# Performance work log

Hardware: AMD Instinct MI355X
Metric: run time of the kernel (lower is better)

The kernel has to match this reference:

```python
import math
import jax, jax.numpy as jnp
import numpy as np

B, LD, LE = 8, 512, 512
D, H, DK, F, L, V = 1024, 16, 64, 4096, 3, 32000
EPS = 1e-5
NEG = -1000000000.0


def setup_inputs() -> dict:
    key = jax.random.key(0)
    ks = jax.random.split(key, 16)
    s = 0.02
    dec_inputs = jax.random.randint(ks[0], (B, LD), 0, V)
    # causal mask: True = masked out (matches masked_fill semantics)
    self_mask = jnp.broadcast_to(jnp.triu(jnp.ones((LD, LD), bool), k=1), (B, LD, LD))
    enc_output = jax.random.normal(ks[1], (B, LE, D), jnp.float32)
    encoder_mask = jnp.zeros((B, LD, LE), bool)  # no encoder padding
    embed = jax.random.normal(ks[2], (V, D), jnp.float32) * s
    # sinusoidal positional encoding, pe[:LD]
    pos = jnp.arange(LD, dtype=jnp.float32)[:, None]
    div = jnp.exp(jnp.arange(0, D, 2, dtype=jnp.float32) * (-math.log(10000.0) / D))
    pe = jnp.zeros((LD, D), jnp.float32)
    pe = pe.at[:, 0::2].set(jnp.sin(pos * div)).at[:, 1::2].set(jnp.cos(pos * div))
    # per-layer params; axis 1 of attn params: 0=self-attn, 1=enc-dec attn
    wq = jax.random.normal(ks[3], (L, 2, D, D), jnp.float32) * s
    wk = jax.random.normal(ks[4], (L, 2, D, D), jnp.float32) * s
    wv = jax.random.normal(ks[5], (L, 2, D, D), jnp.float32) * s
    wo = jax.random.normal(ks[6], (L, 2, D, D), jnp.float32) * s
    bq = jnp.zeros((L, 2, D), jnp.float32)
    bk = jnp.zeros((L, 2, D), jnp.float32)
    bv = jnp.zeros((L, 2, D), jnp.float32)
    bo = jnp.zeros((L, 2, D), jnp.float32)
    ffn_w1 = jax.random.normal(ks[7], (L, F, D), jnp.float32) * s
    ffn_b1 = jnp.zeros((L, F), jnp.float32)
    ffn_w2 = jax.random.normal(ks[8], (L, D, F), jnp.float32) * s
    ffn_b2 = jnp.zeros((L, D), jnp.float32)
    ln_g = jnp.ones((L, 3, D), jnp.float32)   # norm1/2/3 gains
    ln_b = jnp.zeros((L, 3, D), jnp.float32)  # norm1/2/3 biases
    return dict(dec_inputs=dec_inputs, self_mask=self_mask, enc_output=enc_output,
                encoder_mask=encoder_mask, embed=embed, pe=pe,
                wq=wq, bq=bq, wk=wk, bk=bk, wv=wv, bv=bv, wo=wo, bo=bo,
                ffn_w1=ffn_w1, ffn_b1=ffn_b1, ffn_w2=ffn_w2, ffn_b2=ffn_b2,
                ln_g=ln_g, ln_b=ln_b)


def _ln(x, g, b):
    m = jnp.mean(x, axis=-1, keepdims=True)
    v = jnp.mean((x - m) ** 2, axis=-1, keepdims=True)
    return (x - m) * jax.lax.rsqrt(v + EPS) * g + b


def _mha(qi, ki, vi, mask, wq, bq, wk, bk, wv, bv, wo, bo):
    Bq, Lq, _ = qi.shape
    Lk = ki.shape[1]
    Q = (qi @ wq.T + bq).reshape(Bq, Lq, H, DK).transpose(0, 2, 1, 3)
    K = (ki @ wk.T + bk).reshape(Bq, Lk, H, DK).transpose(0, 2, 1, 3)
    Vv = (vi @ wv.T + bv).reshape(Bq, Lk, H, DK).transpose(0, 2, 1, 3)
    scores = jnp.einsum('bhqd,bhkd->bhqk', Q, K) / math.sqrt(DK)
    scores = jnp.where(mask[:, None, :, :], NEG, scores)
    attn = jax.nn.softmax(scores, axis=-1)
    ctx = jnp.einsum('bhqk,bhkd->bhqd', attn, Vv)
    ctx = ctx.transpose(0, 2, 1, 3).reshape(Bq, Lq, H * DK)
    return ctx @ wo.T + bo


def reference(dec_inputs, self_mask, enc_output, encoder_mask, embed, pe,
              wq, bq, wk, bk, wv, bv, wo, bo,
              ffn_w1, ffn_b1, ffn_w2, ffn_b2, ln_g, ln_b):
    x = embed[dec_inputs] * math.sqrt(D) + pe[None, :, :]
    for l in range(L):
        h = _ln(x, ln_g[l, 0], ln_b[l, 0])
        a = _mha(h, h, h, self_mask,
                 wq[l, 0], bq[l, 0], wk[l, 0], bk[l, 0], wv[l, 0], bv[l, 0], wo[l, 0], bo[l, 0])
        x = x + a
        h = _ln(x, ln_g[l, 1], ln_b[l, 1])
        c = _mha(h, enc_output, enc_output, encoder_mask,
                 wq[l, 1], bq[l, 1], wk[l, 1], bk[l, 1], wv[l, 1], bv[l, 1], wo[l, 1], bo[l, 1])
        x = x + c
        h = _ln(x, ln_g[l, 2], ln_b[l, 2])
        f = jax.nn.relu(h @ ffn_w1[l].T + ffn_b1[l]) @ ffn_w2[l].T + ffn_b2[l]
        # faithful quirk of the source: residual is the cross-attn output, not x
        x = c + f
    return x
```

## Files before the change

kernel.cpp:

```cpp
#include <hip/hip_runtime.h>
#include <hip/hip_bf16.h>

using bf16x8 = __attribute__((ext_vector_type(8))) short;
using f32x4  = __attribute__((ext_vector_type(4))) float;
using u16x4  = __attribute__((ext_vector_type(4))) unsigned short;

#define DEVI static __device__ __forceinline__
#define SBAR() asm volatile("s_barrier" ::: "memory")

DEVI unsigned short f2b(float f) {
  unsigned int u = __float_as_uint(f);
  u += 0x7FFFu + ((u >> 16) & 1u);
  return (unsigned short)(u >> 16);
}

DEVI void gload16(const unsigned short* g, unsigned short* l) {
  __builtin_amdgcn_global_load_lds(
      (const __attribute__((address_space(1))) unsigned int*)g,
      (__attribute__((address_space(3))) unsigned int*)l, 16, 0, 0);
}

DEVI float wred_max16(float v) {
#pragma unroll
  for (int m = 1; m < 16; m <<= 1) v = fmaxf(v, __shfl_xor(v, m, 64));
  return v;
}
DEVI float wred_sum16(float v) {
#pragma unroll
  for (int m = 1; m < 16; m <<= 1) v += __shfl_xor(v, m, 64);
  return v;
}


__global__ void cvt_kernel(const float* __restrict__ in,
                           unsigned short* __restrict__ out, int n4) {
  int i = blockIdx.x * blockDim.x + threadIdx.x;
  const int stride = gridDim.x * blockDim.x;
  for (; i < n4; i += stride) {
    const float4 v = ((const float4*)in)[i];
    u16x4 o;
    o[0] = f2b(v.x); o[1] = f2b(v.y); o[2] = f2b(v.z); o[3] = f2b(v.w);
    ((u16x4*)out)[i] = o;
  }
}

__global__ void pack_w(const float* __restrict__ s0,
                       const float* __restrict__ s1,
                       const float* __restrict__ s2,
                       int sub, unsigned short* __restrict__ dst, int nm) {
  const int r = blockIdx.x;
  const int m = blockIdx.y;
  const int l = blockIdx.z;
  const float* src = (m == 0 ? s0 : m == 1 ? s1 : s2)
                   + (size_t)(l * 2 + sub) * 1048576 + (size_t)r * 1024;
  unsigned short* d = dst + ((size_t)(l * nm + m) * 1024 + r) * 1024;
  const int col = threadIdx.x * 4;
  const float4 v = *(const float4*)(src + col);
  u16x4 o;
  o[0] = f2b(v.x); o[1] = f2b(v.y); o[2] = f2b(v.z); o[3] = f2b(v.w);
  *(u16x4*)(d + col) = o;
}

__global__ void pack_bias(const float* __restrict__ s0,
                          const float* __restrict__ s1,
                          const float* __restrict__ s2,
                          int sub, float* __restrict__ dst, int nm) {
  const int m = blockIdx.x, l = blockIdx.y;
  const float* src = (m == 0 ? s0 : m == 1 ? s1 : s2) + (size_t)(l * 2 + sub) * 1024;
  float* d = dst + ((size_t)l * nm + m) * 1024;
  const int i = threadIdx.x * 4;
  *(float4*)(d + i) = *(const float4*)(src + i);
}

__global__ void embed_kernel(const int* __restrict__ ids,
                             const float* __restrict__ emb,
                             const float* __restrict__ pe,
                             float* __restrict__ x) {
  const int row = blockIdx.x;
  const int t = row & 511;
  const int col = threadIdx.x * 4;
  const int id = ids[row];
  const float4 e = *(const float4*)(emb + (size_t)id * 1024 + col);
  const float4 p = *(const float4*)(pe + (size_t)t * 1024 + col);
  float4 o;
  o.x = e.x * 32.f + p.x; o.y = e.y * 32.f + p.y;
  o.z = e.z * 32.f + p.z; o.w = e.w * 32.f + p.w;
  *(float4*)(x + (size_t)row * 1024 + col) = o;
}

__global__ void ln_kernel(const float* __restrict__ x,
                          const float* __restrict__ g,
                          const float* __restrict__ b,
                          unsigned short* __restrict__ out) {
  const int row = blockIdx.x;
  const int l = threadIdx.x;
  const float4* xr = (const float4*)(x + (size_t)row * 1024);
  float4 v[4];
  float s = 0.f;
#pragma unroll
  for (int i = 0; i < 4; ++i) {
    v[i] = xr[l * 4 + i];
    s += v[i].x + v[i].y + v[i].z + v[i].w;
  }
#pragma unroll
  for (int m = 1; m < 64; m <<= 1) s += __shfl_xor(s, m, 64);
  const float mean = s * (1.f / 1024.f);
  float vs = 0.f;
#pragma unroll
  for (int i = 0; i < 4; ++i) {
    float dx = v[i].x - mean, dy = v[i].y - mean, dz = v[i].z - mean, dw = v[i].w - mean;
    vs += dx * dx + dy * dy + dz * dz + dw * dw;
  }
#pragma unroll
  for (int m = 1; m < 64; m <<= 1) vs += __shfl_xor(vs, m, 64);
  const float inv = rsqrtf(vs * (1.f / 1024.f) + 1e-5f);
#pragma unroll
  for (int i = 0; i < 4; ++i) {
    const int col = l * 16 + i * 4;
    const float4 gg = *(const float4*)(g + col);
    const float4 bb = *(const float4*)(b + col);
    u16x4 o;
    o[0] = f2b((v[i].x - mean) * inv * gg.x + bb.x);
    o[1] = f2b((v[i].y - mean) * inv * gg.y + bb.y);
    o[2] = f2b((v[i].z - mean) * inv * gg.z + bb.z);
    o[3] = f2b((v[i].w - mean) * inv * gg.w + bb.w);
    *(u16x4*)(out + (size_t)row * 1024 + col) = o;
  }
}

__global__ void vt_kernel(const unsigned short* __restrict__ Vsrc, int vsd,
                          unsigned short* __restrict__ Vt) {
  __shared__ alignas(16) unsigned short t[64][72];
  const int tt = blockIdx.x;
  const int h  = blockIdx.y;
  const int b  = blockIdx.z;
  const int tid = threadIdx.x;
  const int r  = tid >> 2;
  const int ch = tid & 3;
  const unsigned short* src =
      Vsrc + (size_t)(b * 512 + tt * 64 + r) * vsd + (size_t)h * 64 + ch * 16;
  const bf16x8 v0 = *(const bf16x8*)src;
  const bf16x8 v1 = *(const bf16x8*)(src + 8);
#pragma unroll
  for (int j = 0; j < 8; ++j) {
    t[ch * 16 + j][r]     = (unsigned short)v0[j];
    t[ch * 16 + 8 + j][r] = (unsigned short)v1[j];
  }
  __syncthreads();
  const int d  = tid >> 2;
  const int tp = tid & 3;
  unsigned short* dst = Vt + (((size_t)(b * 16 + h) * 64 + d) * 512) + tt * 64 + tp * 16;
  *(bf16x8*)dst       = *(const bf16x8*)&t[d][tp * 16];
  *(bf16x8*)(dst + 8) = *(const bf16x8*)&t[d][tp * 16 + 8];
}


template<int EPI>
__global__ __launch_bounds__(512, 1) void gemm8p(
    const unsigned short* __restrict__ A,
    const unsigned short* __restrict__ Bw,
    const float* __restrict__ bias,
    int N, unsigned short* __restrict__ out0) {
  constexpr int K = 1024, NT = 16;
  __shared__ alignas(16) unsigned short AsE[256 * 64];
  __shared__ alignas(16) unsigned short BsE[256 * 64];
  __shared__ alignas(16) unsigned short AsO[256 * 64];
  __shared__ alignas(16) unsigned short BsO[256 * 64];
  const int tid = threadIdx.x;
  const int lane = tid & 63;
  const int wave = tid >> 6;
  const int wr = wave >> 2;
  const int wc = wave & 3;
  int id = blockIdx.x;
  const int nwg = gridDim.x;
  id = (id & 7) * (nwg >> 3) + (id >> 3);
  const int nn = N >> 8;
  const int bx = id % nn;
  const int by = id / nn;
  const int m0 = by * 256;
  const int n0 = bx * 256;
  const int ro = lane & 15;
  const int hi = lane >> 4;

  auto stA = [&](unsigned short* buf, int q, int kt) {
    const int row = tid >> 3;
    const int lc = (tid & 7) ^ (row & 7);
    gload16(A + (size_t)(m0 + q * 64 + row) * K + (size_t)kt * 64 + lc * 8,
            buf + q * 4096 + tid * 8);
  };
  auto stB = [&](unsigned short* buf, int q, int kt) {
    const int row = tid >> 3;
    const int lc = (tid & 7) ^ (row & 7);
    gload16(Bw + (size_t)(n0 + q * 64 + row) * K + (size_t)kt * 64 + lc * 8,
            buf + q * 4096 + tid * 8);
  };

  f32x4 acc[8][4];
#pragma unroll
  for (int i = 0; i < 8; ++i)
#pragma unroll
    for (int j = 0; j < 4; ++j) acc[i][j] = f32x4{0.f, 0.f, 0.f, 0.f};

  bf16x8 af[4][2], bfL[2][2], bfR[2][2];

  auto ldAL = [&](const unsigned short* buf) {
#pragma unroll
    for (int mi = 0; mi < 4; ++mi) {
      const int r = wr * 128 + mi * 16 + ro;
#pragma unroll
      for (int ks = 0; ks < 2; ++ks)
        af[mi][ks] = *(const bf16x8*)&buf[r * 64 + (((ks << 2) + hi) ^ (r & 7)) * 8];
    }
  };
  auto ldAH = [&](const unsigned short* buf) {
#pragma unroll
    for (int mi = 0; mi < 4; ++mi) {
      const int r = wr * 128 + 64 + mi * 16 + ro;
#pragma unroll
      for (int ks = 0; ks < 2; ++ks)
        af[mi][ks] = *(const bf16x8*)&buf[r * 64 + (((ks << 2) + hi) ^ (r & 7)) * 8];
    }
  };
  auto ldBL = [&](const unsigned short* buf) {
#pragma unroll
    for (int nj = 0; nj < 2; ++nj) {
      const int r = wc * 64 + nj * 16 + ro;
#pragma unroll
      for (int ks = 0; ks < 2; ++ks)
        bfL[nj][ks] = *(const bf16x8*)&buf[r * 64 + (((ks << 2) + hi) ^ (r & 7)) * 8];
    }
  };
  auto ldBR = [&](const unsigned short* buf) {
#pragma unroll
    for (int nj = 0; nj < 2; ++nj) {
      const int r = wc * 64 + 32 + nj * 16 + ro;
#pragma unroll
      for (int ks = 0; ks < 2; ++ks)
        bfR[nj][ks] = *(const bf16x8*)&buf[r * 64 + (((ks << 2) + hi) ^ (r & 7)) * 8];
    }
  };
  auto mmQ = [&](bf16x8 (&bf)[2][2], int mo, int no) {
    __builtin_amdgcn_s_setprio(1);
#pragma unroll
    for (int ks = 0; ks < 2; ++ks)
#pragma unroll
      for (int mi = 0; mi < 4; ++mi)
#pragma unroll
        for (int nj = 0; nj < 2; ++nj)
          acc[mo + mi][no + nj] =
              __builtin_amdgcn_mfma_f32_16x16x32_bf16(af[mi][ks], bf[nj][ks],
                                                      acc[mo + mi][no + nj], 0, 0, 0);
    __builtin_amdgcn_s_setprio(0);
  };

  stA(AsE, 0, 0); stA(AsE, 1, 0); stA(AsE, 2, 0); stA(AsE, 3, 0);
  stB(BsE, 0, 0); stB(BsE, 1, 0); stB(BsE, 2, 0); stB(BsE, 3, 0);
  stA(AsO, 0, 1); stA(AsO, 1, 1); stA(AsO, 2, 1); stA(AsO, 3, 1);
  stB(BsO, 0, 1); stB(BsO, 1, 1);
  asm volatile("s_waitcnt vmcnt(0)" ::: "memory");
  SBAR();

  for (int t = 0; t < NT; t += 2) {
    const bool last = (t + 2 >= NT);
    ldAL(AsE); ldBL(BsE);
    stB(BsO, 2, t + 1); stB(BsO, 3, t + 1);
    SBAR(); mmQ(bfL, 0, 0); SBAR();
    ldBR(BsE);
    if (!last) { stA(AsE, 0, t + 2); stA(AsE, 2, t + 2); }
    SBAR(); mmQ(bfR, 0, 2); SBAR();
    ldAH(AsE);
    if (!last) { stB(BsE, 0, t + 2); stB(BsE, 1, t + 2); }
    SBAR(); mmQ(bfL, 4, 0); SBAR();
    if (!last) {
      stA(AsE, 1, t + 2); stA(AsE, 3, t + 2);
      asm volatile("s_waitcnt vmcnt(6)" ::: "memory");
    } else {
      asm volatile("s_waitcnt vmcnt(0)" ::: "memory");
    }
    SBAR(); mmQ(bfR, 4, 2); SBAR();
    ldAL(AsO); ldBL(BsO);
    if (!last) { stB(BsE, 2, t + 2); stB(BsE, 3, t + 2); }
    SBAR(); mmQ(bfL, 0, 0); SBAR();
    ldBR(BsO);
    if (!last) { stA(AsO, 0, t + 3); stA(AsO, 2, t + 3); }
    SBAR(); mmQ(bfR, 0, 2); SBAR();
    ldAH(AsO);
    if (!last) { stB(BsO, 0, t + 3); stB(BsO, 1, t + 3); }
    SBAR(); mmQ(bfL, 4, 0); SBAR();
    if (!last) {
      stA(AsO, 1, t + 3); stA(AsO, 3, t + 3);
      asm volatile("s_waitcnt vmcnt(6)" ::: "memory");
    }
    SBAR(); mmQ(bfR, 4, 2); SBAR();
  }

  const int r4 = hi * 4;
#pragma unroll
  for (int mi = 0; mi < 8; ++mi) {
#pragma unroll
    for (int nj = 0; nj < 4; ++nj) {
      const int cg = n0 + wc * 64 + nj * 16 + ro;
      const float bv = bias[cg];
#pragma unroll
      for (int q = 0; q < 4; ++q) {
        const int rg = m0 + wr * 128 + mi * 16 + r4 + q;
        const float v = acc[mi][nj][q] + bv;
        out0[(size_t)rg * N + cg] = f2b(EPI == 1 ? fmaxf(v, 0.f) : v);
      }
    }
  }
}


enum { EPI_BF16 = 0, EPI_RELU_BF16 = 1, EPI_RES = 2, EPI_RES2 = 3 };

template<int EPI, int BM, int BN>
__global__ void gemm_bt(const unsigned short* __restrict__ A,
                        const unsigned short* __restrict__ Bw,
                        const float* __restrict__ bias,
                        int N, int K, int nn,
                        void* out0, const float* res, float* out1) {
  constexpr int MI = BM / 32;
  constexpr int NJ = BN / 32;
  __shared__ alignas(16) unsigned short As[2][BM * 64];
  __shared__ alignas(16) unsigned short Bs[2][BN * 64];
  const int tid = threadIdx.x;
  const int lane = tid & 63;
  const int wave = tid >> 6;
  int id = blockIdx.x;
  const int nwg = gridDim.x;
  id = (id & 7) * (nwg >> 3) + (id >> 3);
  const int bx = id % nn;
  const int by = id / nn;
  const int m0 = by * BM;
  const int n0 = bx * BN;
  const int wm = (wave >> 1) * (BM / 2);
  const int wn = (wave & 1) * (BN / 2);

  auto stage = [&](int buf, int kt) {
    const size_t k0 = (size_t)kt * 64;
#pragma unroll
    for (int i = 0; i < MI; ++i) {
      const int c = tid + 256 * i;
      const int row = c >> 3;
      const int lc = (c & 7) ^ (row & 7);
      gload16(A + (size_t)(m0 + row) * K + k0 + lc * 8, &As[buf][c * 8]);
    }
#pragma unroll
    for (int i = 0; i < NJ; ++i) {
      const int c = tid + 256 * i;
      const int row = c >> 3;
      const int lc = (c & 7) ^ (row & 7);
      gload16(Bw + (size_t)(n0 + row) * K + k0 + lc * 8, &Bs[buf][c * 8]);
    }
  };

  f32x4 acc[MI][NJ];
#pragma unroll
  for (int i = 0; i < MI; ++i)
#pragma unroll
    for (int j = 0; j < NJ; ++j) acc[i][j] = f32x4{0.f, 0.f, 0.f, 0.f};

  const int nk = K >> 6;
  stage(0, 0);
  int cur = 0;
  const int ro = lane & 15;
  const int hi = lane >> 4;
  for (int kt = 0; kt < nk; ++kt) {
    __syncthreads();
    if (kt + 1 < nk) stage(cur ^ 1, kt + 1);
    bf16x8 af[MI][2], bf[NJ][2];
#pragma unroll
    for (int i = 0; i < MI; ++i) {
      const int r = wm + i * 16 + ro;
#pragma unroll
      for (int ks = 0; ks < 2; ++ks)
        af[i][ks] = *(const bf16x8*)&As[cur][r * 64 + (((ks << 2) + hi) ^ (r & 7)) * 8];
    }
#pragma unroll
    for (int j = 0; j < NJ; ++j) {
      const int r = wn + j * 16 + ro;
#pragma unroll
      for (int ks = 0; ks < 2; ++ks)
        bf[j][ks] = *(const bf16x8*)&Bs[cur][r * 64 + (((ks << 2) + hi) ^ (r & 7)) * 8];
    }
#pragma unroll
    for (int ks = 0; ks < 2; ++ks)
#pragma unroll
      for (int i = 0; i < MI; ++i)
#pragma unroll
        for (int j = 0; j < NJ; ++j)
          acc[i][j] = __builtin_amdgcn_mfma_f32_16x16x32_bf16(af[i][ks], bf[j][ks], acc[i][j], 0, 0, 0);
    cur ^= 1;
  }

  const int r4 = hi * 4;
#pragma unroll
  for (int i = 0; i < MI; ++i) {
#pragma unroll
    for (int j = 0; j < NJ; ++j) {
      const int cg = n0 + wn + j * 16 + ro;
      const float bv = bias[cg];
#pragma unroll
      for (int q = 0; q < 4; ++q) {
        const int rg = m0 + wm + i * 16 + r4 + q;
        const size_t idx = (size_t)rg * N + cg;
        const float v = acc[i][j][q] + bv;
        if (EPI == EPI_BF16) {
          ((unsigned short*)out0)[idx] = f2b(v);
        } else if (EPI == EPI_RELU_BF16) {
          ((unsigned short*)out0)[idx] = f2b(fmaxf(v, 0.f));
        } else if (EPI == EPI_RES) {
          ((float*)out0)[idx] = res[idx] + v;
        } else {
          const float r = res[idx];
          ((float*)out0)[idx] = v;
          out1[idx] = r + v;
        }
      }
    }
  }
}


template<bool CAUSAL>
__global__ __launch_bounds__(256) void attn_kernel(
    const unsigned short* __restrict__ Qg, int qs,
    const unsigned short* __restrict__ Kg, int ksd,
    const unsigned short* __restrict__ Vt,
    unsigned short* __restrict__ Og) {
  __shared__ alignas(16) unsigned short Ks[2][64 * 64];
  __shared__ alignas(16) unsigned short Vs[2][64 * 64];
  __shared__ alignas(16) unsigned short Pl[4][32 * 64];
  const int qt0 = blockIdx.x;
  const int h  = blockIdx.y;
  const int b  = blockIdx.z;
  const int tid = threadIdx.x;
  const int lane = tid & 63;
  const int w = tid >> 6;
  const int ro = lane & 15;
  const int hi = lane >> 4;
  const int qrow0 = qt0 * 128 + w * 32;
  const size_t qbase = (size_t)b * 512 * qs  + (size_t)h * 64;
  const size_t kbase = (size_t)b * 512 * ksd + (size_t)h * 64;
  const size_t vbase = ((size_t)(b * 16 + h)) * 64 * 512;
  const size_t obase = (size_t)b * 512 * 1024 + (size_t)h * 64;

  bf16x8 qf[2][2];
#pragma unroll
  for (int mi = 0; mi < 2; ++mi)
#pragma unroll
    for (int ks = 0; ks < 2; ++ks)
      qf[mi][ks] = *(const bf16x8*)&Qg[qbase + (size_t)(qrow0 + mi * 16 + ro) * qs + ks * 32 + hi * 8];

  f32x4 o[2][4];
  float mrun[2][4], lrun[2][4];
#pragma unroll
  for (int mi = 0; mi < 2; ++mi) {
#pragma unroll
    for (int di = 0; di < 4; ++di) o[mi][di] = f32x4{0.f, 0.f, 0.f, 0.f};
#pragma unroll
    for (int q = 0; q < 4; ++q) { mrun[mi][q] = -1e30f; lrun[mi][q] = 0.f; }
  }

  auto stage = [&](int buf, int kt) {
#pragma unroll
    for (int i = 0; i < 2; ++i) {
      const int c = tid + 256 * i;
      const int row = c >> 3;
      const int lc = (c & 7) ^ (row & 7);
      gload16(Kg + kbase + (size_t)(kt * 64 + row) * ksd + lc * 8, &Ks[buf][c * 8]);
    }
#pragma unroll
    for (int i = 0; i < 2; ++i) {
      const int c = tid + 256 * i;
      const int row = c >> 3;
      const int lc = (c & 7) ^ (row & 7);
      gload16(Vt + vbase + (size_t)row * 512 + (size_t)kt * 64 + lc * 8, &Vs[buf][c * 8]);
    }
  };

  const int ktmax = CAUSAL ? (qt0 * 2 + 1) : 7;
  stage(0, 0);
  int cur = 0;
  for (int kt = 0; kt <= ktmax; ++kt) {
    __syncthreads();
    if (kt < ktmax) stage(cur ^ 1, kt + 1);
    const bool skip = CAUSAL && (kt * 64 > qrow0 + 31);
    if (!skip) {
      bf16x8 kf[4][2];
#pragma unroll
      for (int ni = 0; ni < 4; ++ni) {
        const int r = ni * 16 + ro;
#pragma unroll
        for (int ks = 0; ks < 2; ++ks)
          kf[ni][ks] = *(const bf16x8*)&Ks[cur][r * 64 + (((ks << 2) + hi) ^ (r & 7)) * 8];
      }

      f32x4 s[2][4];
#pragma unroll
      for (int mi = 0; mi < 2; ++mi)
#pragma unroll
        for (int ni = 0; ni < 4; ++ni) s[mi][ni] = f32x4{0.f, 0.f, 0.f, 0.f};
#pragma unroll
      for (int ks = 0; ks < 2; ++ks)
#pragma unroll
        for (int mi = 0; mi < 2; ++mi)
#pragma unroll
          for (int ni = 0; ni < 4; ++ni)
            s[mi][ni] = __builtin_amdgcn_mfma_f32_16x16x32_bf16(qf[mi][ks], kf[ni][ks], s[mi][ni], 0, 0, 0);

      const bool dm = CAUSAL && (kt * 64 + 63 > qrow0);
#pragma unroll
      for (int mi = 0; mi < 2; ++mi)
#pragma unroll
        for (int ni = 0; ni < 4; ++ni)
#pragma unroll
          for (int q = 0; q < 4; ++q) {
            float e = s[mi][ni][q] * 0.125f;
            if (dm && (kt * 64 + ni * 16 + ro) > (qrow0 + mi * 16 + hi * 4 + q)) e = -1e9f;
            s[mi][ni][q] = e;
          }

      float fac[2][4];
#pragma unroll
      for (int mi = 0; mi < 2; ++mi)
#pragma unroll
        for (int q = 0; q < 4; ++q) {
          float rm = s[mi][0][q];
#pragma unroll
          for (int ni = 1; ni < 4; ++ni) rm = fmaxf(rm, s[mi][ni][q]);
          rm = wred_max16(rm);
          const float mn = fmaxf(mrun[mi][q], rm);
          fac[mi][q] = __expf(mrun[mi][q] - mn);
          mrun[mi][q] = mn;
        }
#pragma unroll
      for (int mi = 0; mi < 2; ++mi)
#pragma unroll
        for (int q = 0; q < 4; ++q) {
          float rs = 0.f;
#pragma unroll
          for (int ni = 0; ni < 4; ++ni) {
            const float pv = __expf(s[mi][ni][q] - mrun[mi][q]);
            s[mi][ni][q] = pv;
            rs += pv;
          }
          rs = wred_sum16(rs);
          lrun[mi][q] = lrun[mi][q] * fac[mi][q] + rs;
        }
#pragma unroll
      for (int mi = 0; mi < 2; ++mi)
#pragma unroll
        for (int di = 0; di < 4; ++di)
#pragma unroll
          for (int q = 0; q < 4; ++q) o[mi][di][q] *= fac[mi][q];

#pragma unroll
      for (int mi = 0; mi < 2; ++mi)
#pragma unroll
        for (int ni = 0; ni < 4; ++ni)
#pragma unroll
          for (int q = 0; q < 4; ++q) {
            const int row = mi * 16 + hi * 4 + q;
            const int col = ni * 16 + ro;
            const int sc  = ((col >> 3) ^ (row & 7)) * 8 + (col & 7);
            Pl[w][row * 64 + sc] = f2b(s[mi][ni][q]);
          }

      bf16x8 pa[2][2];
#pragma unroll
      for (int mi = 0; mi < 2; ++mi)
#pragma unroll
        for (int ks = 0; ks < 2; ++ks) {
          const int row = mi * 16 + ro;
          pa[mi][ks] = *(const bf16x8*)&Pl[w][row * 64 + (((ks << 2) + hi) ^ (row & 7)) * 8];
        }

#pragma unroll
      for (int di = 0; di < 4; ++di)
#pragma unroll
        for (int ks = 0; ks < 2; ++ks) {
          const int r = di * 16 + ro;
          const bf16x8 vf = *(const bf16x8*)&Vs[cur][r * 64 + (((ks << 2) + hi) ^ (r & 7)) * 8];
#pragma unroll
          for (int mi = 0; mi < 2; ++mi)
            o[mi][di] = __builtin_amdgcn_mfma_f32_16x16x32_bf16(pa[mi][ks], vf, o[mi][di], 0, 0, 0);
        }
    }
    cur ^= 1;
  }

#pragma unroll
  for (int mi = 0; mi < 2; ++mi)
#pragma unroll
    for (int di = 0; di < 4; ++di)
#pragma unroll
      for (int q = 0; q < 4; ++q) {
        const float val = o[mi][di][q] / lrun[mi][q];
        Og[obase + (size_t)(qrow0 + mi * 16 + hi * 4 + q) * 1024 + di * 16 + ro] = f2b(val);
      }
}


extern "C" void kernel_launch(void* const* d_in, const int* in_sizes, int n_in,
                              void* d_out, int out_size, void* d_ws, size_t ws_size,
                              hipStream_t stream) {
  (void)in_sizes; (void)n_in; (void)out_size; (void)ws_size;
  const int*   dec = (const int*)d_in[0];
  const float* enc = (const float*)d_in[2];
  const float* emb = (const float*)d_in[4];
  const float* pe  = (const float*)d_in[5];
  const float* wq  = (const float*)d_in[6];
  const float* bq  = (const float*)d_in[7];
  const float* wk  = (const float*)d_in[8];
  const float* bk  = (const float*)d_in[9];
  const float* wv  = (const float*)d_in[10];
  const float* bv  = (const float*)d_in[11];
  const float* wo  = (const float*)d_in[12];
  const float* bo  = (const float*)d_in[13];
  const float* w1  = (const float*)d_in[14];
  const float* b1  = (const float*)d_in[15];
  const float* w2  = (const float*)d_in[16];
  const float* b2  = (const float*)d_in[17];
  const float* lng = (const float*)d_in[18];
  const float* lnb = (const float*)d_in[19];

  const size_t SZ_ACT = 4194304ull;

  char* p = (char*)d_ws;
  auto alloc = [&](size_t bytes) { char* r = p; p += (bytes + 255) & ~(size_t)255; return r; };
  unsigned short* qkvw  = (unsigned short*)alloc(3ull * 3 * 1048576 * 2);
  unsigned short* kvw   = (unsigned short*)alloc(3ull * 2 * 1048576 * 2);
  unsigned short* wqxb  = (unsigned short*)alloc(3ull * 1048576 * 2);
  unsigned short* Wob   = (unsigned short*)alloc(6291456ull * 2);
  unsigned short* W1b   = (unsigned short*)alloc(12582912ull * 2);
  unsigned short* W2b   = (unsigned short*)alloc(12582912ull * 2);
  unsigned short* encb  = (unsigned short*)alloc(SZ_ACT * 2);
  float*          x     = (float*)alloc(SZ_ACT * 4);
  float*          c     = (float*)alloc(SZ_ACT * 4);
  unsigned short* hb    = (unsigned short*)alloc(SZ_ACT * 2);
  unsigned short* qkvb  = (unsigned short*)alloc(4096ull * 3072 * 2);
  unsigned short* kvb   = (unsigned short*)alloc(4096ull * 6144 * 2);
  unsigned short* qb    = (unsigned short*)alloc(SZ_ACT * 2);
  unsigned short* vtb   = (unsigned short*)alloc(SZ_ACT * 2);
  unsigned short* mid   = (unsigned short*)alloc(4096ull * 4096 * 2);
  float*          qkvbias = (float*)alloc(3ull * 3072 * 4);
  float*          kvbias  = (float*)alloc(3ull * 2048 * 4);

  cvt_kernel<<<2048, 256, 0, stream>>>(wo, Wob, 1572864);
  cvt_kernel<<<2048, 256, 0, stream>>>(w1, W1b, 3145728);
  cvt_kernel<<<2048, 256, 0, stream>>>(w2, W2b, 3145728);
  cvt_kernel<<<2048, 256, 0, stream>>>(enc, encb, 1048576);
  pack_w<<<dim3(1024, 3, 3), 256, 0, stream>>>(wq, wk, wv, 0, qkvw, 3);
  pack_w<<<dim3(1024, 2, 3), 256, 0, stream>>>(wk, wv, wv, 1, kvw, 2);
  pack_w<<<dim3(1024, 1, 3), 256, 0, stream>>>(wq, wq, wq, 1, wqxb, 1);
  pack_bias<<<dim3(3, 3), 256, 0, stream>>>(bq, bk, bv, 0, qkvbias, 3);
  pack_bias<<<dim3(2, 3), 256, 0, stream>>>(bk, bv, bv, 1, kvbias, 2);
  embed_kernel<<<4096, 256, 0, stream>>>(dec, emb, pe, x);

  gemm8p<0><<<16 * 24, 512, 0, stream>>>(encb, kvw, kvbias, 6144, kvb);

  const dim3 gAttn(4, 16, 8);
  const dim3 gVt(8, 16, 8);

  for (int l = 0; l < 3; ++l) {
    const float* g0 = lng + (l * 3 + 0) * 1024; const float* e0 = lnb + (l * 3 + 0) * 1024;
    const float* g1 = lng + (l * 3 + 1) * 1024; const float* e1 = lnb + (l * 3 + 1) * 1024;
    const float* g2 = lng + (l * 3 + 2) * 1024; const float* e2 = lnb + (l * 3 + 2) * 1024;

    ln_kernel<<<4096, 64, 0, stream>>>(x, g0, e0, hb);
    gemm8p<0><<<16 * 12, 512, 0, stream>>>(hb, qkvw + (size_t)l * 3 * 1048576,
        qkvbias + l * 3072, 3072, qkvb);
    vt_kernel<<<gVt, 256, 0, stream>>>(qkvb + 2048, 3072, vtb);
    attn_kernel<true><<<gAttn, 256, 0, stream>>>(qkvb, 3072, qkvb + 1024, 3072, vtb, hb);
    gemm_bt<EPI_RES, 128, 64><<<32 * 16, 256, 0, stream>>>(hb, Wob + (size_t)(l * 2) * 1048576,
        bo + (l * 2) * 1024, 1024, 1024, 16, x, x, nullptr);

    ln_kernel<<<4096, 64, 0, stream>>>(x, g1, e1, hb);
    gemm_bt<EPI_BF16, 128, 64><<<32 * 16, 256, 0, stream>>>(hb, wqxb + (size_t)l * 1048576,
        bq + (l * 2 + 1) * 1024, 1024, 1024, 16, qb, nullptr, nullptr);
    vt_kernel<<<gVt, 256, 0, stream>>>(kvb + l * 2048 + 1024, 6144, vtb);
    attn_kernel<false><<<gAttn, 256, 0, stream>>>(qb, 1024, kvb + l * 2048, 6144, vtb, hb);
    gemm_bt<EPI_RES2, 128, 64><<<32 * 16, 256, 0, stream>>>(hb, Wob + (size_t)(l * 2 + 1) * 1048576,
        bo + (l * 2 + 1) * 1024, 1024, 1024, 16, c, x, x);

    ln_kernel<<<4096, 64, 0, stream>>>(x, g2, e2, hb);
    gemm8p<1><<<16 * 16, 512, 0, stream>>>(hb, W1b + (size_t)l * 4194304,
        b1 + l * 4096, 4096, mid);
    float* xout = (l == 2) ? (float*)d_out : x;
    gemm_bt<EPI_RES, 128, 64><<<32 * 16, 256, 0, stream>>>(mid, W2b + (size_t)l * 4194304,
        b2 + l * 1024, 1024, 4096, 16, xout, c, nullptr);
  }
}
```

Measured before the change: 1.112 ms.

## Split-K the FFN down-projection with the 256x256 GEMM and a reduce kernel

Moves the FFN second GEMM (K=4096, N=1024) from the smaller gemm_bt tile kernel onto the large 256x256 pipelined gemm8p core. It uses a 4-way split-K so the grid fills 256 workgroups. Each split writes fp32 partials to a new buffer, and a separate reduce kernel sums them with the bias and the residual. This adds a 64 MB fp32 partial write and read plus an extra launch in exchange for the higher-throughput GEMM core.

Result: faster. 1.073 ms (-3.6%).

```diff
diff --git a/kernel.cpp b/kernel.cpp
--- a/kernel.cpp
+++ b/kernel.cpp
@@ -155,54 +155,37 @@
 }
 
 
-template<int EPI>
-__global__ __launch_bounds__(512, 1) void gemm8p(
-    const unsigned short* __restrict__ A,
-    const unsigned short* __restrict__ Bw,
-    const float* __restrict__ bias,
-    int N, unsigned short* __restrict__ out0) {
-  constexpr int K = 1024, NT = 16;
-  __shared__ alignas(16) unsigned short AsE[256 * 64];
-  __shared__ alignas(16) unsigned short BsE[256 * 64];
-  __shared__ alignas(16) unsigned short AsO[256 * 64];
-  __shared__ alignas(16) unsigned short BsO[256 * 64];
-  const int tid = threadIdx.x;
+struct G8POut { f32x4 acc[8][4]; int m0, n0, wr, wc, ro, hi; };
+
+template<int LDA, int LDB>
+DEVI void gemm8p_core(const unsigned short* __restrict__ A,
+                      const unsigned short* __restrict__ Bw,
+                      int m0, int n0, int kofs,
+                      unsigned short* AsE, unsigned short* BsE,
+                      unsigned short* AsO, unsigned short* BsO,
+                      int tid, f32x4 (&acc)[8][4]) {
+  constexpr int NT = 16;
   const int lane = tid & 63;
   const int wave = tid >> 6;
   const int wr = wave >> 2;
   const int wc = wave & 3;
-  int id = blockIdx.x;
-  const int nwg = gridDim.x;
-  id = (id & 7) * (nwg >> 3) + (id >> 3);
-  const int nn = N >> 8;
-  const int bx = id % nn;
-  const int by = id / nn;
-  const int m0 = by * 256;
-  const int n0 = bx * 256;
   const int ro = lane & 15;
   const int hi = lane >> 4;
 
   auto stA = [&](unsigned short* buf, int q, int kt) {
     const int row = tid >> 3;
     const int lc = (tid & 7) ^ (row & 7);
-    gload16(A + (size_t)(m0 + q * 64 + row) * K + (size_t)kt * 64 + lc * 8,
+    gload16(A + (size_t)(m0 + q * 64 + row) * LDA + kofs + kt * 64 + lc * 8,
             buf + q * 4096 + tid * 8);
   };
   auto stB = [&](unsigned short* buf, int q, int kt) {
     const int row = tid >> 3;
     const int lc = (tid & 7) ^ (row & 7);
-    gload16(Bw + (size_t)(n0 + q * 64 + row) * K + (size_t)kt * 64 + lc * 8,
+    gload16(Bw + (size_t)(n0 + q * 64 + row) * LDB + kofs + kt * 64 + lc * 8,
             buf + q * 4096 + tid * 8);
   };
 
-  f32x4 acc[8][4];
-#pragma unroll
-  for (int i = 0; i < 8; ++i)
-#pragma unroll
-    for (int j = 0; j < 4; ++j) acc[i][j] = f32x4{0.f, 0.f, 0.f, 0.f};
-
   bf16x8 af[4][2], bfL[2][2], bfR[2][2];
-
   auto ldAL = [&](const unsigned short* buf) {
 #pragma unroll
     for (int mi = 0; mi < 4; ++mi) {
@@ -293,7 +276,40 @@
     }
     SBAR(); mmQ(bfR, 4, 2); SBAR();
   }
-
+}
+
+template<int EPI>
+__global__ __launch_bounds__(512, 1) void gemm8p(
+    const unsigned short* __restrict__ A,
+    const unsigned short* __restrict__ Bw,
+    const float* __restrict__ bias,
+    int N, unsigned short* __restrict__ out0) {
+  __shared__ alignas(16) unsigned short AsE[256 * 64];
+  __shared__ alignas(16) unsigned short BsE[256 * 64];
+  __shared__ alignas(16) unsigned short AsO[256 * 64];
+  __shared__ alignas(16) unsigned short BsO[256 * 64];
+  const int tid = threadIdx.x;
+  int id = blockIdx.x;
+  const int nwg = gridDim.x;
+  id = (id & 7) * (nwg >> 3) + (id >> 3);
+  const int nn = N >> 8;
+  const int bx = id % nn;
+  const int by = id / nn;
+  const int m0 = by * 256;
+  const int n0 = bx * 256;
+
+  f32x4 acc[8][4];
+#pragma unroll
+  for (int i = 0; i < 8; ++i)
+#pragma unroll
+    for (int j = 0; j < 4; ++j) acc[i][j] = f32x4{0.f, 0.f, 0.f, 0.f};
+
+  gemm8p_core<1024, 1024>(A, Bw, m0, n0, 0, AsE, BsE, AsO, BsO, tid, acc);
+
+  const int lane = tid & 63;
+  const int wave = tid >> 6;
+  const int wr = wave >> 2, wc = wave & 3;
+  const int ro = lane & 15, hi = lane >> 4;
   const int r4 = hi * 4;
 #pragma unroll
   for (int mi = 0; mi < 8; ++mi) {
@@ -308,6 +324,79 @@
         out0[(size_t)rg * N + cg] = f2b(EPI == 1 ? fmaxf(v, 0.f) : v);
       }
     }
+  }
+}
+
+__global__ __launch_bounds__(512, 1) void gemm_sk8(
+    const unsigned short* __restrict__ A,
+    const unsigned short* __restrict__ Bw,
+    float* __restrict__ pbuf) {
+  __shared__ alignas(16) unsigned short AsE[256 * 64];
+  __shared__ alignas(16) unsigned short BsE[256 * 64];
+  __shared__ alignas(16) unsigned short AsO[256 * 64];
+  __shared__ alignas(16) unsigned short BsO[256 * 64];
+  const int tid = threadIdx.x;
+  int id = blockIdx.x;
+  const int nwg = gridDim.x;
+  id = (id & 7) * (nwg >> 3) + (id >> 3);
+  const int s  = id >> 6;
+  const int r6 = id & 63;
+  const int bx = r6 & 3;
+  const int by = r6 >> 2;
+  const int m0 = by * 256;
+  const int n0 = bx * 256;
+
+  f32x4 acc[8][4];
+#pragma unroll
+  for (int i = 0; i < 8; ++i)
+#pragma unroll
+    for (int j = 0; j < 4; ++j) acc[i][j] = f32x4{0.f, 0.f, 0.f, 0.f};
+
+  gemm8p_core<4096, 4096>(A, Bw, m0, n0, s * 1024, AsE, BsE, AsO, BsO, tid, acc);
+
+  float* out = pbuf + (size_t)s * 4096 * 1024;
+  const int lane = tid & 63;
+  const int wave = tid >> 6;
+  const int wr = wave >> 2, wc = wave & 3;
+  const int ro = lane & 15, hi = lane >> 4;
+  const int r4 = hi * 4;
+#pragma unroll
+  for (int mi = 0; mi < 8; ++mi)
+#pragma unroll
+    for (int nj = 0; nj < 4; ++nj) {
+      const int cg = n0 + wc * 64 + nj * 16 + ro;
+#pragma unroll
+      for (int q = 0; q < 4; ++q) {
+        const int rg = m0 + wr * 128 + mi * 16 + r4 + q;
+        out[(size_t)rg * 1024 + cg] = acc[mi][nj][q];
+      }
+    }
+}
+
+__global__ void reduce4_kernel(const float* __restrict__ c,
+                               const float* __restrict__ pbuf,
+                               const float* __restrict__ bias,
+                               float* __restrict__ xout) {
+  const int n4 = 4096 * 1024 / 4;
+  int i = blockIdx.x * blockDim.x + threadIdx.x;
+  const int stride = gridDim.x * blockDim.x;
+  const float4* p0 = (const float4*)pbuf;
+  const float4* p1 = (const float4*)(pbuf + 4194304);
+  const float4* p2 = (const float4*)(pbuf + 2 * 4194304);
+  const float4* p3 = (const float4*)(pbuf + 3 * 4194304);
+  for (; i < n4; i += stride) {
+    const float4 cc = ((const float4*)c)[i];
+    const float4 a0 = p0[i];
+    const float4 a1 = p1[i];
+    const float4 a2 = p2[i];
+    const float4 a3 = p3[i];
+    const float4 bb = ((const float4*)bias)[i & 255];
+    float4 o;
+    o.x = cc.x + (a0.x + a1.x) + (a2.x + a3.x) + bb.x;
+    o.y = cc.y + (a0.y + a1.y) + (a2.y + a3.y) + bb.y;
+    o.z = cc.z + (a0.z + a1.z) + (a2.z + a3.z) + bb.z;
+    o.w = cc.w + (a0.w + a1.w) + (a2.w + a3.w) + bb.w;
+    ((float4*)xout)[i] = o;
   }
 }
 
@@ -645,6 +734,7 @@
   unsigned short* qb    = (unsigned short*)alloc(SZ_ACT * 2);
   unsigned short* vtb   = (unsigned short*)alloc(SZ_ACT * 2);
   unsigned short* mid   = (unsigned short*)alloc(4096ull * 4096 * 2);
+  float*          pbuf  = (float*)alloc(4ull * SZ_ACT * 4);
   float*          qkvbias = (float*)alloc(3ull * 3072 * 4);
   float*          kvbias  = (float*)alloc(3ull * 2048 * 4);
 
@@ -688,8 +778,8 @@
     ln_kernel<<<4096, 64, 0, stream>>>(x, g2, e2, hb);
     gemm8p<1><<<16 * 16, 512, 0, stream>>>(hb, W1b + (size_t)l * 4194304,
         b1 + l * 4096, 4096, mid);
+    gemm_sk8<<<256, 512, 0, stream>>>(mid, W2b + (size_t)l * 4194304, pbuf);
     float* xout = (l == 2) ? (float*)d_out : x;
-    gemm_bt<EPI_RES, 128, 64><<<32 * 16, 256, 0, stream>>>(mid, W2b + (size_t)l * 4194304,
-        b2 + l * 1024, 1024, 4096, 16, xout, c, nullptr);
-  }
-}
+    reduce4_kernel<<<2048, 256, 0, stream>>>(c, pbuf, b2 + l * 1024, xout);
+  }
+}
```

## Replace N=1024 GEMMs with 128x128 ping-pong pipelined 8-wave kernel

Applied to the files above, without the earlier changes.

Replaces the simple double-buffered 128x64 gemm_bt used for the output projections, cross-attention Q projection and FFN down-projection with a new gemm4p kernel. The new kernel uses 128x128 tiles, 512 threads, even/odd LDS buffers, interleaved async global-to-LDS loads with explicit vmcnt waits and barriers, and raised wave priority around the MFMA blocks. gemm8p is also split into a reusable core function with a K offset parameter, though that path is not yet used elsewhere. The goal is better overlap of memory and MFMA work and more data reuse per tile, at the cost of fewer workgroups (256) on a large-CU GPU.

New measurement: 1.115 ms. About the same (+0.3%).

```diff
diff --git a/kernel.cpp b/kernel.cpp
--- a/kernel.cpp
+++ b/kernel.cpp
@@ -155,54 +155,35 @@
 }
 
 
-template<int EPI>
-__global__ __launch_bounds__(512, 1) void gemm8p(
-    const unsigned short* __restrict__ A,
-    const unsigned short* __restrict__ Bw,
-    const float* __restrict__ bias,
-    int N, unsigned short* __restrict__ out0) {
-  constexpr int K = 1024, NT = 16;
-  __shared__ alignas(16) unsigned short AsE[256 * 64];
-  __shared__ alignas(16) unsigned short BsE[256 * 64];
-  __shared__ alignas(16) unsigned short AsO[256 * 64];
-  __shared__ alignas(16) unsigned short BsO[256 * 64];
-  const int tid = threadIdx.x;
+template<int LDA, int LDB>
+DEVI void gemm8p_core(const unsigned short* __restrict__ A,
+                      const unsigned short* __restrict__ Bw,
+                      int m0, int n0, int kofs,
+                      unsigned short* AsE, unsigned short* BsE,
+                      unsigned short* AsO, unsigned short* BsO,
+                      int tid, f32x4 (&acc)[8][4]) {
+  constexpr int NT = 16;
   const int lane = tid & 63;
   const int wave = tid >> 6;
   const int wr = wave >> 2;
   const int wc = wave & 3;
-  int id = blockIdx.x;
-  const int nwg = gridDim.x;
-  id = (id & 7) * (nwg >> 3) + (id >> 3);
-  const int nn = N >> 8;
-  const int bx = id % nn;
-  const int by = id / nn;
-  const int m0 = by * 256;
-  const int n0 = bx * 256;
   const int ro = lane & 15;
   const int hi = lane >> 4;
 
   auto stA = [&](unsigned short* buf, int q, int kt) {
     const int row = tid >> 3;
     const int lc = (tid & 7) ^ (row & 7);
-    gload16(A + (size_t)(m0 + q * 64 + row) * K + (size_t)kt * 64 + lc * 8,
+    gload16(A + (size_t)(m0 + q * 64 + row) * LDA + kofs + kt * 64 + lc * 8,
             buf + q * 4096 + tid * 8);
   };
   auto stB = [&](unsigned short* buf, int q, int kt) {
     const int row = tid >> 3;
     const int lc = (tid & 7) ^ (row & 7);
-    gload16(Bw + (size_t)(n0 + q * 64 + row) * K + (size_t)kt * 64 + lc * 8,
+    gload16(Bw + (size_t)(n0 + q * 64 + row) * LDB + kofs + kt * 64 + lc * 8,
             buf + q * 4096 + tid * 8);
   };
 
-  f32x4 acc[8][4];
-#pragma unroll
-  for (int i = 0; i < 8; ++i)
-#pragma unroll
-    for (int j = 0; j < 4; ++j) acc[i][j] = f32x4{0.f, 0.f, 0.f, 0.f};
-
   bf16x8 af[4][2], bfL[2][2], bfR[2][2];
-
   auto ldAL = [&](const unsigned short* buf) {
 #pragma unroll
     for (int mi = 0; mi < 4; ++mi) {
@@ -293,7 +274,40 @@
     }
     SBAR(); mmQ(bfR, 4, 2); SBAR();
   }
-
+}
+
+template<int EPI>
+__global__ __launch_bounds__(512, 1) void gemm8p(
+    const unsigned short* __restrict__ A,
+    const unsigned short* __restrict__ Bw,
+    const float* __restrict__ bias,
+    int N, unsigned short* __restrict__ out0) {
+  __shared__ alignas(16) unsigned short AsE[256 * 64];
+  __shared__ alignas(16) unsigned short BsE[256 * 64];
+  __shared__ alignas(16) unsigned short AsO[256 * 64];
+  __shared__ alignas(16) unsigned short BsO[256 * 64];
+  const int tid = threadIdx.x;
+  int id = blockIdx.x;
+  const int nwg = gridDim.x;
+  id = (id & 7) * (nwg >> 3) + (id >> 3);
+  const int nn = N >> 8;
+  const int bx = id % nn;
+  const int by = id / nn;
+  const int m0 = by * 256;
+  const int n0 = bx * 256;
+
+  f32x4 acc[8][4];
+#pragma unroll
+  for (int i = 0; i < 8; ++i)
+#pragma unroll
+    for (int j = 0; j < 4; ++j) acc[i][j] = f32x4{0.f, 0.f, 0.f, 0.f};
+
+  gemm8p_core<1024, 1024>(A, Bw, m0, n0, 0, AsE, BsE, AsO, BsO, tid, acc);
+
+  const int lane = tid & 63;
+  const int wave = tid >> 6;
+  const int wr = wave >> 2, wc = wave & 3;
+  const int ro = lane & 15, hi = lane >> 4;
   const int r4 = hi * 4;
 #pragma unroll
   for (int mi = 0; mi < 8; ++mi) {
@@ -314,98 +328,131 @@
 
 enum { EPI_BF16 = 0, EPI_RELU_BF16 = 1, EPI_RES = 2, EPI_RES2 = 3 };
 
-template<int EPI, int BM, int BN>
-__global__ void gemm_bt(const unsigned short* __restrict__ A,
-                        const unsigned short* __restrict__ Bw,
-                        const float* __restrict__ bias,
-                        int N, int K, int nn,
-                        void* out0, const float* res, float* out1) {
-  constexpr int MI = BM / 32;
-  constexpr int NJ = BN / 32;
-  __shared__ alignas(16) unsigned short As[2][BM * 64];
-  __shared__ alignas(16) unsigned short Bs[2][BN * 64];
+template<int EPI>
+__global__ __launch_bounds__(512, 2) void gemm4p(
+    const unsigned short* __restrict__ A,
+    const unsigned short* __restrict__ Bw,
+    const float* __restrict__ bias,
+    int N, int K, int nn,
+    void* out0, const float* res, float* out1) {
+  __shared__ alignas(16) unsigned short AsE[128 * 64];
+  __shared__ alignas(16) unsigned short BsE[128 * 64];
+  __shared__ alignas(16) unsigned short AsO[128 * 64];
+  __shared__ alignas(16) unsigned short BsO[128 * 64];
   const int tid = threadIdx.x;
   const int lane = tid & 63;
   const int wave = tid >> 6;
+  const int wr = wave >> 1;
+  const int wc = wave & 1;
   int id = blockIdx.x;
   const int nwg = gridDim.x;
   id = (id & 7) * (nwg >> 3) + (id >> 3);
   const int bx = id % nn;
   const int by = id / nn;
-  const int m0 = by * BM;
-  const int n0 = bx * BN;
-  const int wm = (wave >> 1) * (BM / 2);
-  const int wn = (wave & 1) * (BN / 2);
-
-  auto stage = [&](int buf, int kt) {
-    const size_t k0 = (size_t)kt * 64;
-#pragma unroll
-    for (int i = 0; i < MI; ++i) {
-      const int c = tid + 256 * i;
-      const int row = c >> 3;
-      const int lc = (c & 7) ^ (row & 7);
-      gload16(A + (size_t)(m0 + row) * K + k0 + lc * 8, &As[buf][c * 8]);
-    }
-#pragma unroll
-    for (int i = 0; i < NJ; ++i) {
-      const int c = tid + 256 * i;
-      const int row = c >> 3;
-      const int lc = (c & 7) ^ (row & 7);
-      gload16(Bw + (size_t)(n0 + row) * K + k0 + lc * 8, &Bs[buf][c * 8]);
-    }
-  };
-
-  f32x4 acc[MI][NJ];
-#pragma unroll
-  for (int i = 0; i < MI; ++i)
-#pragma unroll
-    for (int j = 0; j < NJ; ++j) acc[i][j] = f32x4{0.f, 0.f, 0.f, 0.f};
-
-  const int nk = K >> 6;
-  stage(0, 0);
-  int cur = 0;
+  const int m0 = by * 128;
+  const int n0 = bx * 128;
   const int ro = lane & 15;
   const int hi = lane >> 4;
-  for (int kt = 0; kt < nk; ++kt) {
-    __syncthreads();
-    if (kt + 1 < nk) stage(cur ^ 1, kt + 1);
-    bf16x8 af[MI][2], bf[NJ][2];
-#pragma unroll
-    for (int i = 0; i < MI; ++i) {
-      const int r = wm + i * 16 + ro;
+
+  auto stA = [&](unsigned short* buf, int h, int kt) {
+    const int row = tid >> 3;
+    const int lc = (tid & 7) ^ (row & 7);
+    gload16(A + (size_t)(m0 + h * 64 + row) * K + (size_t)kt * 64 + lc * 8,
+            buf + h * 4096 + tid * 8);
+  };
+  auto stB = [&](unsigned short* buf, int h, int kt) {
+    const int row = tid >> 3;
+    const int lc = (tid & 7) ^ (row & 7);
+    gload16(Bw + (size_t)(n0 + h * 64 + row) * K + (size_t)kt * 64 + lc * 8,
+            buf + h * 4096 + tid * 8);
+  };
+
+  f32x4 acc[2][4];
+#pragma unroll
+  for (int i = 0; i < 2; ++i)
+#pragma unroll
+    for (int j = 0; j < 4; ++j) acc[i][j] = f32x4{0.f, 0.f, 0.f, 0.f};
+
+  bf16x8 af[2][2], bfL[2][2], bfR[2][2];
+  auto ldA = [&](const unsigned short* buf) {
+#pragma unroll
+    for (int mi = 0; mi < 2; ++mi) {
+      const int r = wr * 32 + mi * 16 + ro;
 #pragma unroll
       for (int ks = 0; ks < 2; ++ks)
-        af[i][ks] = *(const bf16x8*)&As[cur][r * 64 + (((ks << 2) + hi) ^ (r & 7)) * 8];
-    }
-#pragma unroll
-    for (int j = 0; j < NJ; ++j) {
-      const int r = wn + j * 16 + ro;
+        af[mi][ks] = *(const bf16x8*)&buf[r * 64 + (((ks << 2) + hi) ^ (r & 7)) * 8];
+    }
+  };
+  auto ldBL = [&](const unsigned short* buf) {
+#pragma unroll
+    for (int nj = 0; nj < 2; ++nj) {
+      const int r = wc * 64 + nj * 16 + ro;
 #pragma unroll
       for (int ks = 0; ks < 2; ++ks)
-        bf[j][ks] = *(const bf16x8*)&Bs[cur][r * 64 + (((ks << 2) + hi) ^ (r & 7)) * 8];
-    }
+        bfL[nj][ks] = *(const bf16x8*)&buf[r * 64 + (((ks << 2) + hi) ^ (r & 7)) * 8];
+    }
+  };
+  auto ldBR = [&](const unsigned short* buf) {
+#pragma unroll
+    for (int nj = 0; nj < 2; ++nj) {
+      const int r = wc * 64 + 32 + nj * 16 + ro;
+#pragma unroll
+      for (int ks = 0; ks < 2; ++ks)
+        bfR[nj][ks] = *(const bf16x8*)&buf[r * 64 + (((ks << 2) + hi) ^ (r & 7)) * 8];
+    }
+  };
+  auto mmH = [&](bf16x8 (&bf)[2][2], int no) {
+    __builtin_amdgcn_s_setprio(1);
 #pragma unroll
     for (int ks = 0; ks < 2; ++ks)
 #pragma unroll
-      for (int i = 0; i < MI; ++i)
-#pragma unroll
-        for (int j = 0; j < NJ; ++j)
-          acc[i][j] = __builtin_amdgcn_mfma_f32_16x16x32_bf16(af[i][ks], bf[j][ks], acc[i][j], 0, 0, 0);
-    cur ^= 1;
+      for (int mi = 0; mi < 2; ++mi)
+#pragma unroll
+        for (int nj = 0; nj < 2; ++nj)
+          acc[mi][no + nj] =
+              __builtin_amdgcn_mfma_f32_16x16x32_bf16(af[mi][ks], bf[nj][ks],
+                                                      acc[mi][no + nj], 0, 0, 0);
+    __builtin_amdgcn_s_setprio(0);
+  };
+
+  const int NT = K >> 6;
+  stA(AsE, 0, 0); stA(AsE, 1, 0);
+  stB(BsE, 0, 0); stB(BsE, 1, 0);
+  stA(AsO, 0, 1); stA(AsO, 1, 1);
+  asm volatile("s_waitcnt vmcnt(0)" ::: "memory");
+  SBAR();
+
+  for (int t = 0; t < NT; t += 2) {
+    const bool s2 = (t + 2 < NT), s3 = (t + 3 < NT);
+    ldA(AsE); ldBL(BsE);
+    stB(BsO, 0, t + 1); stB(BsO, 1, t + 1);
+    SBAR(); mmH(bfL, 0); SBAR();
+    ldBR(BsE);
+    if (s2) { stA(AsE, 0, t + 2); stA(AsE, 1, t + 2); }
+    asm volatile("s_waitcnt vmcnt(2)" ::: "memory");
+    SBAR(); mmH(bfR, 2); SBAR();
+    ldA(AsO); ldBL(BsO);
+    if (s2) { stB(BsE, 0, t + 2); stB(BsE, 1, t + 2); }
+    SBAR(); mmH(bfL, 0); SBAR();
+    ldBR(BsO);
+    if (s3) { stA(AsO, 0, t + 3); stA(AsO, 1, t + 3); }
+    if (s2) asm volatile("s_waitcnt vmcnt(2)" ::: "memory");
+    else    asm volatile("s_waitcnt vmcnt(0)" ::: "memory");
+    SBAR(); mmH(bfR, 2); SBAR();
   }
 
   const int r4 = hi * 4;
 #pragma unroll
-  for (int i = 0; i < MI; ++i) {
-#pragma unroll
-    for (int j = 0; j < NJ; ++j) {
-      const int cg = n0 + wn + j * 16 + ro;
+  for (int mi = 0; mi < 2; ++mi) {
+#pragma unroll
+    for (int nj = 0; nj < 4; ++nj) {
+      const int cg = n0 + wc * 64 + nj * 16 + ro;
       const float bv = bias[cg];
 #pragma unroll
       for (int q = 0; q < 4; ++q) {
-        const int rg = m0 + wm + i * 16 + r4 + q;
+        const int rg = m0 + wr * 32 + mi * 16 + r4 + q;
         const size_t idx = (size_t)rg * N + cg;
-        const float v = acc[i][j][q] + bv;
+        const float v = acc[mi][nj][q] + bv;
         if (EPI == EPI_BF16) {
           ((unsigned short*)out0)[idx] = f2b(v);
         } else if (EPI == EPI_RELU_BF16) {
@@ -674,22 +721,22 @@
         qkvbias + l * 3072, 3072, qkvb);
     vt_kernel<<<gVt, 256, 0, stream>>>(qkvb + 2048, 3072, vtb);
     attn_kernel<true><<<gAttn, 256, 0, stream>>>(qkvb, 3072, qkvb + 1024, 3072, vtb, hb);
-    gemm_bt<EPI_RES, 128, 64><<<32 * 16, 256, 0, stream>>>(hb, Wob + (size_t)(l * 2) * 1048576,
-        bo + (l * 2) * 1024, 1024, 1024, 16, x, x, nullptr);
+    gemm4p<EPI_RES><<<32 * 8, 512, 0, stream>>>(hb, Wob + (size_t)(l * 2) * 1048576,
+        bo + (l * 2) * 1024, 1024, 1024, 8, x, x, nullptr);
 
     ln_kernel<<<4096, 64, 0, stream>>>(x, g1, e1, hb);
-    gemm_bt<EPI_BF16, 128, 64><<<32 * 16, 256, 0, stream>>>(hb, wqxb + (size_t)l * 1048576,
-        bq + (l * 2 + 1) * 1024, 1024, 1024, 16, qb, nullptr, nullptr);
+    gemm4p<EPI_BF16><<<32 * 8, 512, 0, stream>>>(hb, wqxb + (size_t)l * 1048576,
+        bq + (l * 2 + 1) * 1024, 1024, 1024, 8, qb, nullptr, nullptr);
     vt_kernel<<<gVt, 256, 0, stream>>>(kvb + l * 2048 + 1024, 6144, vtb);
     attn_kernel<false><<<gAttn, 256, 0, stream>>>(qb, 1024, kvb + l * 2048, 6144, vtb, hb);
-    gemm_bt<EPI_RES2, 128, 64><<<32 * 16, 256, 0, stream>>>(hb, Wob + (size_t)(l * 2 + 1) * 1048576,
-        bo + (l * 2 + 1) * 1024, 1024, 1024, 16, c, x, x);
+    gemm4p<EPI_RES2><<<32 * 8, 512, 0, stream>>>(hb, Wob + (size_t)(l * 2 + 1) * 1048576,
+        bo + (l * 2 + 1) * 1024, 1024, 1024, 8, c, x, x);
 
     ln_kernel<<<4096, 64, 0, stream>>>(x, g2, e2, hb);
     gemm8p<1><<<16 * 16, 512, 0, stream>>>(hb, W1b + (size_t)l * 4194304,
         b1 + l * 4096, 4096, mid);
     float* xout = (l == 2) ? (float*)d_out : x;
-    gemm_bt<EPI_RES, 128, 64><<<32 * 16, 256, 0, stream>>>(mid, W2b + (size_t)l * 4194304,
-        b2 + l * 1024, 1024, 4096, 16, xout, c, nullptr);
-  }
-}
+    gemm4p<EPI_RES><<<32 * 8, 512, 0, stream>>>(mid, W2b + (size_t)l * 4194304,
+        b2 + l * 1024, 1024, 4096, 8, xout, c, nullptr);
+  }
+}
```
